# Kernel tuning notes

Measured on AMD Instinct MI355X. Metric: run time of the kernel, lower is better.

Reference implementation:

```python
import jax, jax.numpy as jnp
import numpy as np

B, T, E, H = 8, 2048, 1024, 64

def setup_inputs() -> dict:
    key = jax.random.key(0)
    kx, kk, kq, kv = jax.random.split(key, 4)
    x = jax.random.normal(kx, (B, T, E), dtype=jnp.float32)
    # nn.Linear weight init scale ~ 1/sqrt(fan_in); use small normal weights
    s = 1.0 / np.sqrt(E)
    Wk = jax.random.normal(kk, (E, H), dtype=jnp.float32) * s
    Wq = jax.random.normal(kq, (E, H), dtype=jnp.float32) * s
    Wv = jax.random.normal(kv, (E, H), dtype=jnp.float32) * s
    return {"x": x, "Wk": Wk, "Wq": Wq, "Wv": Wv}

def reference(x, Wk, Wq, Wv):
    # x: [B,T,E]; projections to head_size H
    k = jnp.einsum('bte,eh->bth', x, Wk)
    q = jnp.einsum('bte,eh->bth', x, Wq)
    v = jnp.einsum('bte,eh->bth', x, Wv)
    # NOTE: original scales by num_embds**-0.5 (E, not head_size)
    scale = jnp.asarray(E, x.dtype) ** -0.5
    wei = jnp.einsum('bqh,bkh->bqk', q, k) * scale  # [B,T,T]
    causal = jnp.tril(jnp.ones((T, T), dtype=bool))
    wei = jnp.where(causal, wei, -jnp.inf)
    wei = jax.nn.softmax(wei, axis=-1)
    # dropout p=0.0 -> identity (eval-mode deterministic baseline)
    out = jnp.einsum('bqk,bkh->bqh', wei, v)  # [B,T,H]
    return out
```

## Files before the change

kernel.cpp:

```cpp
#include <hip/hip_runtime.h>
#include <hip/hip_bf16.h>

#define B_ 8
#define T_ 2048
#define E_ 1024
#define H_ 64

typedef __attribute__((ext_vector_type(8))) short short8v;
typedef __attribute__((ext_vector_type(4))) float f32x4;

__device__ __forceinline__ unsigned short bfbits(float f) {
  return __builtin_bit_cast(unsigned short, __float2bfloat16(f));
}

__global__ __launch_bounds__(256) void prep_wf(
    const float* __restrict__ Wk, const float* __restrict__ Wq,
    const float* __restrict__ Wv, __hip_bfloat16* __restrict__ Wf) {
  const int idx = blockIdx.x * 256 + threadIdx.x;
  const int f = idx >> 9;
  const int e = idx & 511;
  const int l = e >> 3, j = e & 7;
  const int cf = f >> 5, kb = f & 31;
  const int m = cf >> 2;
  const int c = (cf & 3) * 16 + (l & 15);
  const int k = kb * 32 + (l >> 4) * 8 + j;
  const float* W = (m == 0) ? Wk : (m == 1) ? Wq : Wv;
  float v = W[k * H_ + c];
  if (m == 1) v *= 0.03125f;
  Wf[idx] = __float2bfloat16(v);
}

__global__ __launch_bounds__(512) void proj_mfma(
    const float* __restrict__ x, const __hip_bfloat16* __restrict__ Wf,
    __hip_bfloat16* __restrict__ Qb, __hip_bfloat16* __restrict__ Kb,
    __hip_bfloat16* __restrict__ Vt) {
  __shared__ __hip_bfloat16 xp[32 * 128 * 8];
  __shared__ __hip_bfloat16 rep[8][16][24];
  const int tid = threadIdx.x;
  const int lane = tid & 63;
  const int w = tid >> 6;
  const int rowg = w >> 2;
  const int colh = w & 3;
  const int r = lane & 15, g = lane >> 4;
  const int r0 = blockIdx.x * 32;

  {
    const int row = tid >> 4;
    const int ci = tid & 15;
    const float* src = x + (size_t)(r0 + row) * E_ + ci * 8;
    char* dst = (char*)xp + row * 2048;
    #pragma unroll
    for (int j = 0; j < 8; ++j) {
      const f32x4 lo = *(const f32x4*)(src + j * 128);
      const f32x4 hi = *(const f32x4*)(src + j * 128 + 4);
      short8v t8;
      t8[0] = (short)bfbits(lo[0]); t8[1] = (short)bfbits(lo[1]);
      t8[2] = (short)bfbits(lo[2]); t8[3] = (short)bfbits(lo[3]);
      t8[4] = (short)bfbits(hi[0]); t8[5] = (short)bfbits(hi[1]);
      t8[6] = (short)bfbits(hi[2]); t8[7] = (short)bfbits(hi[3]);
      const int sl = ci + 16 * j;
      const int ss = (sl & 120) | ((sl & 7) ^ (row & 7));
      *(short8v*)(dst + ss * 16) = t8;
    }
  }
  __syncthreads();

  f32x4 acc[3];
  #pragma unroll
  for (int m = 0; m < 3; ++m) acc[m] = (f32x4){0.f, 0.f, 0.f, 0.f};

  const int arow = rowg * 16 + r;
  const char* abase = (const char*)xp + arow * 2048;

  short8v WA[6], WB[6];
  auto loadW = [&](int t, short8v (&Wn)[6]) {
    #pragma unroll
    for (int m = 0; m < 3; ++m)
      #pragma unroll
      for (int h = 0; h < 2; ++h)
        Wn[m * 2 + h] = *(const short8v*)(
            Wf + (((size_t)(m * 4 + colh) * 32 + t * 2 + h) << 9) + lane * 8);
  };
  auto computeT = [&](int t, short8v (&Wc)[6]) {
    #pragma unroll
    for (int kh = 0; kh < 2; ++kh) {
      const int slot = t * 8 + kh * 4 + g;
      const int ss = (slot & 120) | ((slot & 7) ^ (arow & 7));
      const short8v A = *(const short8v*)(abase + ss * 16);
      #pragma unroll
      for (int m = 0; m < 3; ++m)
        acc[m] = __builtin_amdgcn_mfma_f32_16x16x32_bf16(A, Wc[m * 2 + kh], acc[m], 0, 0, 0);
    }
  };

  loadW(0, WA);
  #pragma unroll
  for (int t = 0; t < 16; t += 2) {
    if (t + 1 < 16) loadW(t + 1, WB);
    computeT(t, WA);
    if (t + 2 < 16) loadW(t + 2, WA);
    computeT(t + 1, WB);
  }

  __hip_bfloat16* rp = &rep[w][0][0];
  #pragma unroll
  for (int m = 0; m < 2; ++m) {
    __hip_bfloat16* Pout = (m == 0) ? Kb : Qb;
    #pragma unroll
    for (int reg = 0; reg < 4; ++reg)
      rp[(g * 4 + reg) * 24 + r] = __float2bfloat16(acc[m][reg]);
    asm volatile("s_waitcnt lgkmcnt(0)" ::: "memory");
    __builtin_amdgcn_sched_barrier(0);
    if (lane < 32) {
      const int row = lane >> 1, ch = lane & 1;
      *(uint4*)(Pout + (size_t)(r0 + rowg * 16 + row) * H_ + colh * 16 + ch * 8) =
          *(const uint4*)(rp + row * 24 + ch * 8);
    }
    asm volatile("s_waitcnt lgkmcnt(0)" ::: "memory");
    __builtin_amdgcn_sched_barrier(0);
  }
  const int b = r0 >> 11;
  const int tt = (r0 & 2047) + rowg * 16 + g * 4;
  ushort4 pk;
  pk.x = bfbits(acc[2][0]); pk.y = bfbits(acc[2][1]);
  pk.z = bfbits(acc[2][2]); pk.w = bfbits(acc[2][3]);
  *(ushort4*)(Vt + (size_t)(b * 64 + colh * 16 + r) * T_ + tt) = pk;
}

__global__ __launch_bounds__(128, 2) void attn_mfma(
    const __hip_bfloat16* __restrict__ Qb, const __hip_bfloat16* __restrict__ Kb,
    const __hip_bfloat16* __restrict__ Vt, float* __restrict__ out) {
  __shared__ __hip_bfloat16 Ps[2][16][72];
  __shared__ float cmb[64][20];
  __shared__ float ml[16][2];
  const int tid = threadIdx.x;
  const int lane = tid & 63;
  const int w = tid >> 6;
  const int r = lane & 15, g = lane >> 4;
  const int blk = blockIdx.x;
  const int b = blk & 7;
  const int i = blk >> 3;
  const int s_ = i >> 5, j_ = i & 31;
  const int qt = (s_ == 0) ? j_ : (s_ == 1) ? (63 - j_) : (s_ == 2) ? (64 + j_) : (127 - j_);
  const int q0 = qt * 16;
  const size_t tb = (size_t)b * T_;
  const int bb = b * 64;

  const short8v qf0 = *(const short8v*)(Qb + (tb + q0 + r) * H_ + g * 8);
  const short8v qf1 = *(const short8v*)(Qb + (tb + q0 + r) * H_ + 32 + g * 8);

  f32x4 o[4];
  #pragma unroll
  for (int k2 = 0; k2 < 4; ++k2) o[k2] = (f32x4){0.f, 0.f, 0.f, 0.f};
  float mrun = -1e30f, lrun = 0.f;

  const int nt = (qt >> 2) + 1;
  const int h_ = (nt + 1) >> 1;
  const int t0 = w ? h_ : 0;
  const int t1 = w ? nt : h_;

  short8v kbA[4][2], kbB[4][2];
  auto loadK = [&](int t, short8v (&kb)[4][2]) {
    #pragma unroll
    for (int kg = 0; kg < 4; ++kg)
      #pragma unroll
      for (int c = 0; c < 2; ++c)
        kb[kg][c] = *(const short8v*)(Kb + (tb + t * 64 + kg * 16 + r) * H_ + c * 32 + g * 8);
  };

  auto body = [&](int t, short8v (&kbU)[4][2], short8v (&kbP)[4][2]) {
    short8v vb[4][2];
    #pragma unroll
    for (int hg = 0; hg < 4; ++hg)
      #pragma unroll
      for (int c = 0; c < 2; ++c)
        vb[hg][c] = *(const short8v*)(
            Vt + (size_t)(bb + hg * 16 + r) * T_ + t * 64 + c * 32 + g * 8);
    if (t + 1 < t1) loadK(t + 1, kbP);

    f32x4 s[4];
    #pragma unroll
    for (int k2 = 0; k2 < 4; ++k2) s[k2] = (f32x4){0.f, 0.f, 0.f, 0.f};
    __builtin_amdgcn_s_setprio(1);
    #pragma unroll
    for (int kg = 0; kg < 4; ++kg) {
      s[kg] = __builtin_amdgcn_mfma_f32_16x16x32_bf16(kbU[kg][0], qf0, s[kg], 0, 0, 0);
      s[kg] = __builtin_amdgcn_mfma_f32_16x16x32_bf16(kbU[kg][1], qf1, s[kg], 0, 0, 0);
    }
    __builtin_amdgcn_s_setprio(0);

    if (t == nt - 1) {
      #pragma unroll
      for (int kg = 0; kg < 4; ++kg)
        #pragma unroll
        for (int reg = 0; reg < 4; ++reg)
          if (t * 64 + kg * 16 + g * 4 + reg > q0 + r) s[kg][reg] = -1e30f;
    }

    float pm = s[0][0];
    #pragma unroll
    for (int kg = 0; kg < 4; ++kg)
      #pragma unroll
      for (int reg = 0; reg < 4; ++reg) pm = fmaxf(pm, s[kg][reg]);
    pm = fmaxf(pm, __shfl_xor(pm, 16));
    pm = fmaxf(pm, __shfl_xor(pm, 32));
    const float nm = fmaxf(mrun, pm);
    const float al = __expf(mrun - nm);
    mrun = nm;
    float p[4][4];
    float rs = 0.f;
    #pragma unroll
    for (int kg = 0; kg < 4; ++kg)
      #pragma unroll
      for (int reg = 0; reg < 4; ++reg) {
        p[kg][reg] = __expf(s[kg][reg] - nm);
        rs += p[kg][reg];
      }
    rs += __shfl_xor(rs, 16);
    rs += __shfl_xor(rs, 32);
    lrun = lrun * al + rs;
    #pragma unroll
    for (int hg = 0; hg < 4; ++hg) o[hg] *= al;

    #pragma unroll
    for (int kg = 0; kg < 4; ++kg) {
      ushort4 u;
      u.x = bfbits(p[kg][0]); u.y = bfbits(p[kg][1]);
      u.z = bfbits(p[kg][2]); u.w = bfbits(p[kg][3]);
      *(ushort4*)&Ps[w][r][kg * 16 + g * 4] = u;
    }
    short8v pf[2];
    pf[0] = *(const short8v*)&Ps[w][r][g * 8];
    pf[1] = *(const short8v*)&Ps[w][r][32 + g * 8];

    __builtin_amdgcn_s_setprio(1);
    #pragma unroll
    for (int c = 0; c < 2; ++c)
      #pragma unroll
      for (int hg = 0; hg < 4; ++hg)
        o[hg] = __builtin_amdgcn_mfma_f32_16x16x32_bf16(vb[hg][c], pf[c], o[hg], 0, 0, 0);
    __builtin_amdgcn_s_setprio(0);
  };

  if (t0 < t1) {
    loadK(t0, kbA);
    int t = t0;
    while (true) {
      body(t, kbA, kbB);
      if (++t >= t1) break;
      body(t, kbB, kbA);
      if (++t >= t1) break;
    }
  }

  if (w == 1) {
    if (g == 0) { ml[r][0] = mrun; ml[r][1] = lrun; }
    #pragma unroll
    for (int hg = 0; hg < 4; ++hg) *(f32x4*)&cmb[lane][hg * 4] = o[hg];
  }
  __syncthreads();
  if (w == 0) {
    const float m1 = ml[r][0], l1 = ml[r][1];
    const float mm = fmaxf(mrun, m1);
    const float sc0 = __expf(mrun - mm), sc1 = __expf(m1 - mm);
    const float inv = 1.f / (lrun * sc0 + l1 * sc1);
    #pragma unroll
    for (int hg = 0; hg < 4; ++hg) {
      const f32x4 o1 = *(const f32x4*)&cmb[lane][hg * 4];
      f32x4 res = (o[hg] * sc0 + o1 * sc1) * inv;
      *(f32x4*)(out + (tb + q0 + r) * H_ + hg * 16 + g * 4) = res;
    }
  }
}

extern "C" void kernel_launch(void* const* d_in, const int* in_sizes, int n_in,
                              void* d_out, int out_size, void* d_ws, size_t ws_size,
                              hipStream_t stream) {
  const float* x  = (const float*)d_in[0];
  const float* Wk = (const float*)d_in[1];
  const float* Wq = (const float*)d_in[2];
  const float* Wv = (const float*)d_in[3];
  float* out = (float*)d_out;

  __hip_bfloat16* Qb = (__hip_bfloat16*)d_ws;
  __hip_bfloat16* Kb = Qb + (size_t)B_ * T_ * H_;
  __hip_bfloat16* Vt = Kb + (size_t)B_ * T_ * H_;
  __hip_bfloat16* Wf = Vt + (size_t)B_ * T_ * H_;

  prep_wf<<<(12 * 32 * 512) / 256, 256, 0, stream>>>(Wk, Wq, Wv, Wf);
  proj_mfma<<<(B_ * T_) / 32, 512, 0, stream>>>(x, Wf, Qb, Kb, Vt);
  attn_mfma<<<B_ * (T_ / 16), 128, 0, stream>>>(Qb, Kb, Vt, out);
}
```

Measured before the change: 67.37 us.

## Split projection per matrix and stream x from global with register prefetch

The projection kernel no longer stages a 32-row tile of x into shared memory and computes K, Q and V together. Each block now handles one of the three matrices for 16 rows. Each wave reads x directly from global memory, converting to bf16 in registers with a 3-deep prefetch pipeline. This raises block count and removes LDS staging and the barrier. The cost is that x is re-read for each matrix and by each wave within a block, which depends on cache hits.

```diff
diff --git a/kernel.cpp b/kernel.cpp
--- a/kernel.cpp
+++ b/kernel.cpp
@@ -30,101 +30,73 @@
   Wf[idx] = __float2bfloat16(v);
 }
 
-__global__ __launch_bounds__(512) void proj_mfma(
+__global__ __launch_bounds__(256) void proj_mfma(
     const float* __restrict__ x, const __hip_bfloat16* __restrict__ Wf,
     __hip_bfloat16* __restrict__ Qb, __hip_bfloat16* __restrict__ Kb,
     __hip_bfloat16* __restrict__ Vt) {
-  __shared__ __hip_bfloat16 xp[32 * 128 * 8];
-  __shared__ __hip_bfloat16 rep[8][16][24];
+  __shared__ __hip_bfloat16 rep[4][16][24];
   const int tid = threadIdx.x;
   const int lane = tid & 63;
   const int w = tid >> 6;
-  const int rowg = w >> 2;
-  const int colh = w & 3;
   const int r = lane & 15, g = lane >> 4;
-  const int r0 = blockIdx.x * 32;
-
-  {
-    const int row = tid >> 4;
-    const int ci = tid & 15;
-    const float* src = x + (size_t)(r0 + row) * E_ + ci * 8;
-    char* dst = (char*)xp + row * 2048;
-    #pragma unroll
-    for (int j = 0; j < 8; ++j) {
-      const f32x4 lo = *(const f32x4*)(src + j * 128);
-      const f32x4 hi = *(const f32x4*)(src + j * 128 + 4);
-      short8v t8;
-      t8[0] = (short)bfbits(lo[0]); t8[1] = (short)bfbits(lo[1]);
-      t8[2] = (short)bfbits(lo[2]); t8[3] = (short)bfbits(lo[3]);
-      t8[4] = (short)bfbits(hi[0]); t8[5] = (short)bfbits(hi[1]);
-      t8[6] = (short)bfbits(hi[2]); t8[7] = (short)bfbits(hi[3]);
-      const int sl = ci + 16 * j;
-      const int ss = (sl & 120) | ((sl & 7) ^ (row & 7));
-      *(short8v*)(dst + ss * 16) = t8;
-    }
-  }
-  __syncthreads();
-
-  f32x4 acc[3];
+  const int mg = blockIdx.x >> 10;
+  const int rt = blockIdx.x & 1023;
+  const int r0 = rt * 16;
+  const int c0 = w * 16;
+  const int cf = mg * 4 + w;
+
+  f32x4 acc = (f32x4){0.f, 0.f, 0.f, 0.f};
+  const float* xr = x + (size_t)(r0 + r) * E_ + g * 8;
+  const __hip_bfloat16* wfb = Wf + ((size_t)cf << 14) + lane * 8;
+
+  f32x4 aL[4], aH[4];
+  short8v bS[4];
+  auto loadA = [&](int s, int kb) {
+    aL[s] = *(const f32x4*)(xr + kb * 32);
+    aH[s] = *(const f32x4*)(xr + kb * 32 + 4);
+  };
+  auto loadB = [&](int s, int kb) {
+    bS[s] = *(const short8v*)(wfb + (kb << 9));
+  };
+  auto step = [&](int s) {
+    short8v A;
+    A[0] = (short)bfbits(aL[s][0]); A[1] = (short)bfbits(aL[s][1]);
+    A[2] = (short)bfbits(aL[s][2]); A[3] = (short)bfbits(aL[s][3]);
+    A[4] = (short)bfbits(aH[s][0]); A[5] = (short)bfbits(aH[s][1]);
+    A[6] = (short)bfbits(aH[s][2]); A[7] = (short)bfbits(aH[s][3]);
+    acc = __builtin_amdgcn_mfma_f32_16x16x32_bf16(A, bS[s], acc, 0, 0, 0);
+  };
+
+  loadA(0, 0); loadB(0, 0);
+  loadA(1, 1); loadB(1, 1);
+  loadA(2, 2); loadB(2, 2);
   #pragma unroll
-  for (int m = 0; m < 3; ++m) acc[m] = (f32x4){0.f, 0.f, 0.f, 0.f};
-
-  const int arow = rowg * 16 + r;
-  const char* abase = (const char*)xp + arow * 2048;
-
-  short8v WA[6], WB[6];
-  auto loadW = [&](int t, short8v (&Wn)[6]) {
-    #pragma unroll
-    for (int m = 0; m < 3; ++m)
-      #pragma unroll
-      for (int h = 0; h < 2; ++h)
-        Wn[m * 2 + h] = *(const short8v*)(
-            Wf + (((size_t)(m * 4 + colh) * 32 + t * 2 + h) << 9) + lane * 8);
-  };
-  auto computeT = [&](int t, short8v (&Wc)[6]) {
-    #pragma unroll
-    for (int kh = 0; kh < 2; ++kh) {
-      const int slot = t * 8 + kh * 4 + g;
-      const int ss = (slot & 120) | ((slot & 7) ^ (arow & 7));
-      const short8v A = *(const short8v*)(abase + ss * 16);
-      #pragma unroll
-      for (int m = 0; m < 3; ++m)
-        acc[m] = __builtin_amdgcn_mfma_f32_16x16x32_bf16(A, Wc[m * 2 + kh], acc[m], 0, 0, 0);
-    }
-  };
-
-  loadW(0, WA);
-  #pragma unroll
-  for (int t = 0; t < 16; t += 2) {
-    if (t + 1 < 16) loadW(t + 1, WB);
-    computeT(t, WA);
-    if (t + 2 < 16) loadW(t + 2, WA);
-    computeT(t + 1, WB);
-  }
-
-  __hip_bfloat16* rp = &rep[w][0][0];
-  #pragma unroll
-  for (int m = 0; m < 2; ++m) {
-    __hip_bfloat16* Pout = (m == 0) ? Kb : Qb;
+  for (int t = 0; t < 32; ++t) {
+    if (t + 3 < 32) { loadA((t + 3) & 3, t + 3); loadB((t + 3) & 3, t + 3); }
+    step(t & 3);
+  }
+
+  if (mg < 2) {
+    __hip_bfloat16* Pout = (mg == 0) ? Kb : Qb;
+    __hip_bfloat16* rp = &rep[w][0][0];
     #pragma unroll
     for (int reg = 0; reg < 4; ++reg)
-      rp[(g * 4 + reg) * 24 + r] = __float2bfloat16(acc[m][reg]);
+      rp[(g * 4 + reg) * 24 + r] = __float2bfloat16(acc[reg]);
     asm volatile("s_waitcnt lgkmcnt(0)" ::: "memory");
     __builtin_amdgcn_sched_barrier(0);
     if (lane < 32) {
       const int row = lane >> 1, ch = lane & 1;
-      *(uint4*)(Pout + (size_t)(r0 + rowg * 16 + row) * H_ + colh * 16 + ch * 8) =
+      *(uint4*)(Pout + (size_t)(r0 + row) * H_ + c0 + ch * 8) =
           *(const uint4*)(rp + row * 24 + ch * 8);
     }
-    asm volatile("s_waitcnt lgkmcnt(0)" ::: "memory");
-    __builtin_amdgcn_sched_barrier(0);
-  }
-  const int b = r0 >> 11;
-  const int tt = (r0 & 2047) + rowg * 16 + g * 4;
-  ushort4 pk;
-  pk.x = bfbits(acc[2][0]); pk.y = bfbits(acc[2][1]);
-  pk.z = bfbits(acc[2][2]); pk.w = bfbits(acc[2][3]);
-  *(ushort4*)(Vt + (size_t)(b * 64 + colh * 16 + r) * T_ + tt) = pk;
+  } else {
+    const int b = r0 >> 11;
+    const int tt = (r0 & 2047) + g * 4;
+    ushort4 pk;
+    pk.x = bfbits(acc[0]); pk.y = bfbits(acc[1]);
+    pk.z = bfbits(acc[2]); pk.w = bfbits(acc[3]);
+    *(ushort4*)(Vt + (size_t)(b * 64 + c0 + r) * T_ + tt) = pk;
+  }
 }
 
 __global__ __launch_bounds__(128, 2) void attn_mfma(
@@ -288,6 +260,6 @@
   __hip_bfloat16* Wf = Vt + (size_t)B_ * T_ * H_;
 
   prep_wf<<<(12 * 32 * 512) / 256, 256, 0, stream>>>(Wk, Wq, Wv, Wf);
-  proj_mfma<<<(B_ * T_) / 32, 512, 0, stream>>>(x, Wf, Qb, Kb, Vt);
+  proj_mfma<<<3 * 1024, 256, 0, stream>>>(x, Wf, Qb, Kb, Vt);
   attn_mfma<<<B_ * (T_ / 16), 128, 0, stream>>>(Qb, Kb, Vt, out);
 }
```

Result: slower. 138.6 us (+105.7%).
